# Kernel optimization log

Hardware: AMD Instinct MI355X
Metric: run time of the kernel (lower is better)

## Reference

```python
import jax, jax.numpy as jnp
import numpy as np

N_NODES = 100000
N_IN = 256
N_OUT = 64
N_EDGES = 1600000


def setup_inputs() -> dict:
    key = jax.random.key(0)
    k_x, k_w, k_b, k_v, k_r, k_c = jax.random.split(key, 6)
    x = jax.random.normal(k_x, (N_NODES, N_IN), dtype=jnp.float32)
    W = jax.random.normal(k_w, (N_IN, N_OUT), dtype=jnp.float32) * (1.0 / np.sqrt(N_IN))
    b = jax.random.normal(k_b, (N_OUT,), dtype=jnp.float32) * 0.01
    adj_vals = jax.random.uniform(k_v, (N_EDGES,), dtype=jnp.float32)
    edge_rows = jax.random.randint(k_r, (N_EDGES,), 0, N_NODES, dtype=jnp.int32)
    edge_cols = jax.random.randint(k_c, (N_EDGES,), 0, N_NODES, dtype=jnp.int32)
    return {"x": x, "W": W, "b": b, "adj_vals": adj_vals,
            "edge_rows": edge_rows, "edge_cols": edge_cols}


def reference(x, W, b, adj_vals, edge_rows, edge_cols):
    # linear projection: [N, n_in] @ [n_in, n_out] + b -> [N, n_out]
    h = x @ W + b
    # sparse-dense matmul: out[i] = sum_e adj_vals[e] * h[edge_cols[e]] for edge_rows[e]==i
    msgs = h[edge_cols] * adj_vals[:, None]  # [E, n_out]
    out = jax.ops.segment_sum(msgs, edge_rows, num_segments=N_NODES)
    return out
```

## Files before the change

### kernel.cpp

```cpp
#include <hip/hip_runtime.h>


#include <stdint.h>

constexpr int KDIM = 256;
constexpr int MOUT = 64;

constexpr int RPB = 128;
constexpr int RPB_SHIFT = 7;
constexpr int MAXBUCK = 1024;
constexpr int CHUNK = 8192;
constexpr int COL_BITS = 20;
constexpr int COL_MASK = (1 << COL_BITS) - 1;
constexpr int SORT_CAP = 6144;

typedef __attribute__((ext_vector_type(8))) short short8v;
typedef __attribute__((ext_vector_type(4))) float f32x4;

__device__ __forceinline__ unsigned short f2bf(float f) {
  unsigned u = __float_as_uint(f);
  return (unsigned short)((u + 0x7fffu + ((u >> 16) & 1u)) >> 16);
}

__global__ __launch_bounds__(256)
void wt_transpose(const float* __restrict__ W, unsigned short* __restrict__ wt) {
  int n = blockIdx.x;
  int k = threadIdx.x;
  wt[n * KDIM + k] = f2bf(W[(size_t)k * MOUT + n]);
}

__global__ __launch_bounds__(256)
void gemm_mfma(const float* __restrict__ x, const unsigned short* __restrict__ wt,
               const float* __restrict__ bvec, unsigned short* __restrict__ h, int N) {
  __shared__ unsigned short wlds[MOUT][264];

  const int t = threadIdx.x;
  for (int i = t; i < MOUT * 32; i += 256) {
    int n = i >> 5, seg = i & 31;
    uint4 v = *reinterpret_cast<const uint4*>(&wt[n * KDIM + seg * 8]);
    *reinterpret_cast<uint4*>(&wlds[n][seg * 8]) = v;
  }
  __syncthreads();

  const int wave = t >> 6, lane = t & 63;
  const int lo = lane & 15, hi = lane >> 4;
  const int rowbase = blockIdx.x * 128 + wave * 32;

  float bias[4];
#pragma unroll
  for (int nt = 0; nt < 4; ++nt) bias[nt] = bvec[nt * 16 + lo];

  f32x4 acc[2][4] = {};

#pragma unroll
  for (int ks = 0; ks < 8; ++ks) {
    short8v bfr[4];
#pragma unroll
    for (int nt = 0; nt < 4; ++nt)
      bfr[nt] = *reinterpret_cast<const short8v*>(&wlds[nt * 16 + lo][ks * 32 + hi * 8]);
#pragma unroll
    for (int mr = 0; mr < 2; ++mr) {
      int r = rowbase + mr * 16 + lo;
      if (r >= N) r = N - 1;
      const float* xp = &x[(size_t)r * KDIM + ks * 32 + hi * 8];
      float4 p0 = *reinterpret_cast<const float4*>(xp);
      float4 p1 = *reinterpret_cast<const float4*>(xp + 4);
      short8v a;
      a[0] = (short)f2bf(p0.x); a[1] = (short)f2bf(p0.y);
      a[2] = (short)f2bf(p0.z); a[3] = (short)f2bf(p0.w);
      a[4] = (short)f2bf(p1.x); a[5] = (short)f2bf(p1.y);
      a[6] = (short)f2bf(p1.z); a[7] = (short)f2bf(p1.w);
#pragma unroll
      for (int nt = 0; nt < 4; ++nt)
        acc[mr][nt] = __builtin_amdgcn_mfma_f32_16x16x32_bf16(a, bfr[nt], acc[mr][nt], 0, 0, 0);
    }
  }

#pragma unroll
  for (int mr = 0; mr < 2; ++mr)
#pragma unroll
    for (int reg = 0; reg < 4; ++reg) {
      int row = rowbase + mr * 16 + hi * 4 + reg;
      if (row < N) {
#pragma unroll
        for (int nt = 0; nt < 4; ++nt)
          h[(size_t)row * MOUT + nt * 16 + lo] = f2bf(acc[mr][nt][reg] + bias[nt]);
      }
    }
}

__global__ __launch_bounds__(256)
void bucket_hist(const int* __restrict__ rows, int* __restrict__ bcnt, int E, int nbuck) {
  __shared__ int cnt[MAXBUCK];
  for (int i = threadIdx.x; i < nbuck; i += 256) cnt[i] = 0;
  __syncthreads();
  for (int e = blockIdx.x * 256 + threadIdx.x; e < E; e += gridDim.x * 256)
    atomicAdd(&cnt[rows[e] >> RPB_SHIFT], 1);
  __syncthreads();
  for (int i = threadIdx.x; i < nbuck; i += 256)
    if (cnt[i]) atomicAdd(&bcnt[i], cnt[i]);
}

__global__ __launch_bounds__(1024)
void scan_buckets(const int* __restrict__ bcnt, int* __restrict__ bptr,
                  int* __restrict__ bcur, int nbuck, int E) {
  __shared__ int buf[1024];
  int t = threadIdx.x;
  int x = (t < nbuck) ? bcnt[t] : 0;
  buf[t] = x;
  __syncthreads();
#pragma unroll
  for (int off = 1; off < 1024; off <<= 1) {
    int v = (t >= off) ? buf[t - off] : 0;
    __syncthreads();
    buf[t] += v;
    __syncthreads();
  }
  if (t < nbuck) {
    int ex = buf[t] - x;
    bptr[t] = ex;
    bcur[t] = ex;
  }
  if (t == 0) bptr[nbuck] = E;
}

__global__ __launch_bounds__(256)
void bucket_scatter(const int* __restrict__ rows, const int* __restrict__ cols,
                    const float* __restrict__ vals, int* __restrict__ bcur,
                    int2* __restrict__ sorted, int E, int nbuck) {
  __shared__ int lcnt[MAXBUCK];
  __shared__ int lbase[MAXBUCK];
  const int t = threadIdx.x;
  const int e0 = blockIdx.x * CHUNK;
  const int e1 = min(e0 + CHUNK, E);

  for (int i = t; i < nbuck; i += 256) lcnt[i] = 0;
  __syncthreads();
  for (int e = e0 + t; e < e1; e += 256)
    atomicAdd(&lcnt[rows[e] >> RPB_SHIFT], 1);
  __syncthreads();
  for (int i = t; i < nbuck; i += 256) {
    int c = lcnt[i];
    lbase[i] = c ? atomicAdd(&bcur[i], c) : 0;
  }
  __syncthreads();
  for (int i = t; i < nbuck; i += 256) lcnt[i] = 0;
  __syncthreads();
  for (int e = e0 + t; e < e1; e += 256) {
    int r = rows[e];
    int b = r >> RPB_SHIFT;
    int lrow = r & (RPB - 1);
    int pos = lbase[b] + atomicAdd(&lcnt[b], 1);
    sorted[pos] = make_int2((lrow << COL_BITS) | cols[e], __float_as_int(vals[e]));
  }
}

__global__ __launch_bounds__(256)
void bucket_sort(int2* __restrict__ sorted, const int* __restrict__ bptr,
                 int* __restrict__ row_ptr, int* __restrict__ bflag,
                 int N, int E, int nbuck) {
  __shared__ int2 eds[SORT_CAP];
  __shared__ int lcnt[RPB];
  __shared__ int loff[RPB];
  __shared__ int lcur[RPB];
  const int t = threadIdx.x;
  const int b = blockIdx.x;
  const int s = bptr[b];
  const int e = bptr[b + 1];
  const int cnt = e - s;
  const int row0 = b << RPB_SHIFT;

  if (b == 0 && t == 0) row_ptr[N] = E;

  if (cnt > SORT_CAP) {
    if (t == 0) bflag[b] = 1;
    if (t < RPB && row0 + t < N) row_ptr[row0 + t] = s;
    return;
  }
  if (t == 0) bflag[b] = 0;

  if (t < RPB) lcnt[t] = 0;
  __syncthreads();
  for (int j = s + t; j < e; j += 256) {
    int2 p = sorted[j];
    eds[j - s] = p;
    atomicAdd(&lcnt[p.x >> COL_BITS], 1);
  }
  __syncthreads();
  if (t < RPB) loff[t] = lcnt[t];
  __syncthreads();
  for (int off = 1; off < RPB; off <<= 1) {
    int v = (t < RPB && t >= off) ? loff[t - off] : 0;
    __syncthreads();
    if (t < RPB) loff[t] += v;
    __syncthreads();
  }
  if (t < RPB) {
    int ex = loff[t] - lcnt[t];
    loff[t] = ex;
    lcur[t] = 0;
    int grow = row0 + t;
    if (grow < N) row_ptr[grow] = s + ex;
  }
  __syncthreads();
  for (int idx = t; idx < cnt; idx += 256) {
    int2 p = eds[idx];
    int lr = p.x >> COL_BITS;
    int pos = s + loff[lr] + atomicAdd(&lcur[lr], 1);
    sorted[pos] = p;
  }
}

__device__ __forceinline__ void edge_fma(float* acc, const unsigned short* h,
                                         int2 p, int part) {
  float v = __int_as_float(p.y);
  int col = p.x & COL_MASK;
  uint4 hv = *reinterpret_cast<const uint4*>(&h[(size_t)col * MOUT + part * 8]);
  acc[0] += v * __uint_as_float(hv.x << 16);
  acc[1] += v * __uint_as_float(hv.x & 0xffff0000u);
  acc[2] += v * __uint_as_float(hv.y << 16);
  acc[3] += v * __uint_as_float(hv.y & 0xffff0000u);
  acc[4] += v * __uint_as_float(hv.z << 16);
  acc[5] += v * __uint_as_float(hv.z & 0xffff0000u);
  acc[6] += v * __uint_as_float(hv.w << 16);
  acc[7] += v * __uint_as_float(hv.w & 0xffff0000u);
}

__global__ __launch_bounds__(256)
void reduce_rows(const unsigned short* __restrict__ h, const int2* __restrict__ sorted,
                 const int* __restrict__ row_ptr, const int* __restrict__ bptr,
                 const int* __restrict__ bflag, float* __restrict__ out, int N) {
  int row = (blockIdx.x * 256 + threadIdx.x) >> 6;
  if (row >= N) return;
  int lane = threadIdx.x & 63;
  int slot = lane >> 3;
  int part = lane & 7;
  int b = row >> RPB_SHIFT;
  int lrow = row & (RPB - 1);
  bool filt = bflag[b] != 0;

  float acc[8];
#pragma unroll
  for (int i = 0; i < 8; ++i) acc[i] = 0.f;

  if (!filt) {
    int s = row_ptr[row];
    int e = row_ptr[row + 1];
    int j = s + slot;
    for (; j + 8 < e; j += 16) {
      int2 p0 = sorted[j];
      int2 p1 = sorted[j + 8];
      float v0 = __int_as_float(p0.y);
      float v1 = __int_as_float(p1.y);
      const uint4* a0 = reinterpret_cast<const uint4*>(
          &h[(size_t)(p0.x & COL_MASK) * MOUT + part * 8]);
      const uint4* a1 = reinterpret_cast<const uint4*>(
          &h[(size_t)(p1.x & COL_MASK) * MOUT + part * 8]);
      uint4 h0 = *a0;
      uint4 h1 = *a1;
      acc[0] += v0 * __uint_as_float(h0.x << 16);
      acc[1] += v0 * __uint_as_float(h0.x & 0xffff0000u);
      acc[2] += v0 * __uint_as_float(h0.y << 16);
      acc[3] += v0 * __uint_as_float(h0.y & 0xffff0000u);
      acc[4] += v0 * __uint_as_float(h0.z << 16);
      acc[5] += v0 * __uint_as_float(h0.z & 0xffff0000u);
      acc[6] += v0 * __uint_as_float(h0.w << 16);
      acc[7] += v0 * __uint_as_float(h0.w & 0xffff0000u);
      acc[0] += v1 * __uint_as_float(h1.x << 16);
      acc[1] += v1 * __uint_as_float(h1.x & 0xffff0000u);
      acc[2] += v1 * __uint_as_float(h1.y << 16);
      acc[3] += v1 * __uint_as_float(h1.y & 0xffff0000u);
      acc[4] += v1 * __uint_as_float(h1.z << 16);
      acc[5] += v1 * __uint_as_float(h1.z & 0xffff0000u);
      acc[6] += v1 * __uint_as_float(h1.w << 16);
      acc[7] += v1 * __uint_as_float(h1.w & 0xffff0000u);
    }
    if (j < e) edge_fma(acc, h, sorted[j], part);
  } else {
    int s = bptr[b];
    int e = bptr[b + 1];
    for (int j = s + slot; j < e; j += 8) {
      int2 p = sorted[j];
      if ((p.x >> COL_BITS) != lrow) continue;
      edge_fma(acc, h, p, part);
    }
  }

#pragma unroll
  for (int m = 8; m <= 32; m <<= 1)
#pragma unroll
    for (int i = 0; i < 8; ++i)
      acc[i] += __shfl_xor(acc[i], m, 64);

  if (slot == 0) {
    float* op = &out[(size_t)row * MOUT + part * 8];
    *reinterpret_cast<float4*>(op)     = make_float4(acc[0], acc[1], acc[2], acc[3]);
    *reinterpret_cast<float4*>(op + 4) = make_float4(acc[4], acc[5], acc[6], acc[7]);
  }
}

__global__ __launch_bounds__(256)
void scatter_edges(const unsigned short* __restrict__ h, const float* __restrict__ vals,
                   const int* __restrict__ rows, const int* __restrict__ cols,
                   float* __restrict__ out, int E) {
  long long idx = (long long)blockIdx.x * blockDim.x + threadIdx.x;
  int e = (int)(idx >> 4);
  int part = (int)(idx & 15);
  if (e >= E) return;
  int r = rows[e];
  int c = cols[e];
  float v = vals[e];
  uint2 hv = *reinterpret_cast<const uint2*>(&h[(size_t)c * MOUT + part * 4]);
  float* op = &out[(size_t)r * MOUT + part * 4];
  atomicAdd(op + 0, v * __uint_as_float(hv.x << 16));
  atomicAdd(op + 1, v * __uint_as_float(hv.x & 0xffff0000u));
  atomicAdd(op + 2, v * __uint_as_float(hv.y << 16));
  atomicAdd(op + 3, v * __uint_as_float(hv.y & 0xffff0000u));
}

static inline size_t align256(size_t x) { return (x + 255) & ~(size_t)255; }

extern "C" void kernel_launch(void* const* d_in, const int* in_sizes, int n_in,
                              void* d_out, int out_size, void* d_ws, size_t ws_size,
                              hipStream_t stream) {
  const float* x    = (const float*)d_in[0];
  const float* W    = (const float*)d_in[1];
  const float* bvec = (const float*)d_in[2];
  const float* vals = (const float*)d_in[3];
  const int* erows  = (const int*)d_in[4];
  const int* ecols  = (const int*)d_in[5];
  float* out = (float*)d_out;

  const int N = in_sizes[0] / KDIM;
  const int E = in_sizes[3];
  const int nbuck = (N + RPB - 1) / RPB;

  char* ws = (char*)d_ws;
  size_t off_h  = 0;
  size_t off_wt = align256(off_h + (size_t)N * MOUT * sizeof(short));
  size_t off_bp = align256(off_wt + (size_t)MOUT * KDIM * sizeof(short));
  size_t off_bc = align256(off_bp + (size_t)(nbuck + 1) * sizeof(int));
  size_t off_cu = align256(off_bc + (size_t)nbuck * sizeof(int));
  size_t off_bf = align256(off_cu + (size_t)nbuck * sizeof(int));
  size_t off_rp = align256(off_bf + (size_t)nbuck * sizeof(int));
  size_t off_sp = align256(off_rp + (size_t)(N + 1) * sizeof(int));
  size_t need   = off_sp + (size_t)E * sizeof(int2);

  unsigned short* h  = (unsigned short*)(ws + off_h);
  unsigned short* wt = (unsigned short*)(ws + off_wt);

  dim3 blk256(256);
  wt_transpose<<<dim3(MOUT), blk256, 0, stream>>>(W, wt);
  gemm_mfma<<<dim3((N + 127) / 128), blk256, 0, stream>>>(x, wt, bvec, h, N);

  if (ws_size >= need && nbuck <= MAXBUCK && N < (1 << COL_BITS)) {
    int* bptr  = (int*)(ws + off_bp);
    int* bcnt  = (int*)(ws + off_bc);
    int* bcur  = (int*)(ws + off_cu);
    int* bflag = (int*)(ws + off_bf);
    int* row_ptr = (int*)(ws + off_rp);
    int2* sorted = (int2*)(ws + off_sp);

    hipMemsetAsync(bcnt, 0, (size_t)nbuck * sizeof(int), stream);
    bucket_hist<<<dim3(256), blk256, 0, stream>>>(erows, bcnt, E, nbuck);
    scan_buckets<<<dim3(1), dim3(1024), 0, stream>>>(bcnt, bptr, bcur, nbuck, E);
    bucket_scatter<<<dim3((E + CHUNK - 1) / CHUNK), blk256, 0, stream>>>(
        erows, ecols, vals, bcur, sorted, E, nbuck);
    bucket_sort<<<dim3(nbuck), blk256, 0, stream>>>(sorted, bptr, row_ptr, bflag, N, E, nbuck);
    reduce_rows<<<dim3(((size_t)N * 64 + 255) / 256), blk256, 0, stream>>>(
        h, sorted, row_ptr, bptr, bflag, out, N);
  } else {
    hipMemsetAsync(d_out, 0, (size_t)out_size * sizeof(float), stream);
    long long work = (long long)E * 16;
    scatter_edges<<<dim3((unsigned)((work + 255) / 256)), blk256, 0, stream>>>(h, vals, erows, ecols, out, E);
  }
}
```

Before: 144.5 us.

## Fuse weight transpose into histogram kernel and GEMM into bucket scatter launch

The W transpose is merged into the bucket histogram kernel as extra blocks, and the MFMA projection GEMM is merged with the edge bucket scatter into one launch, with blocks picking their role by index and sharing one LDS buffer. This removes two kernel launches and lets the compute-heavy GEMM blocks run alongside the memory-bound scatter blocks. The scan kernel is also generalized to loop over chunks of 1024 buckets. The cost is higher LDS use per block for the scatter role and uneven work across block roles.

```diff
diff --git a/kernel.cpp b/kernel.cpp
--- a/kernel.cpp
+++ b/kernel.cpp
@@ -13,6 +13,7 @@
 constexpr int COL_BITS = 20;
 constexpr int COL_MASK = (1 << COL_BITS) - 1;
 constexpr int SORT_CAP = 6144;
+constexpr int HIST_BLOCKS = 256;
 
 typedef __attribute__((ext_vector_type(8))) short short8v;
 typedef __attribute__((ext_vector_type(4))) float f32x4;
@@ -23,81 +24,22 @@
 }
 
 __global__ __launch_bounds__(256)
-void wt_transpose(const float* __restrict__ W, unsigned short* __restrict__ wt) {
-  int n = blockIdx.x;
-  int k = threadIdx.x;
-  wt[n * KDIM + k] = f2bf(W[(size_t)k * MOUT + n]);
-}
-
-__global__ __launch_bounds__(256)
-void gemm_mfma(const float* __restrict__ x, const unsigned short* __restrict__ wt,
-               const float* __restrict__ bvec, unsigned short* __restrict__ h, int N) {
-  __shared__ unsigned short wlds[MOUT][264];
-
+void prep(const float* __restrict__ W, unsigned short* __restrict__ wt,
+          const int* __restrict__ rows, int* __restrict__ bcnt, int E, int nbuck) {
   const int t = threadIdx.x;
-  for (int i = t; i < MOUT * 32; i += 256) {
-    int n = i >> 5, seg = i & 31;
-    uint4 v = *reinterpret_cast<const uint4*>(&wt[n * KDIM + seg * 8]);
-    *reinterpret_cast<uint4*>(&wlds[n][seg * 8]) = v;
-  }
-  __syncthreads();
-
-  const int wave = t >> 6, lane = t & 63;
-  const int lo = lane & 15, hi = lane >> 4;
-  const int rowbase = blockIdx.x * 128 + wave * 32;
-
-  float bias[4];
-#pragma unroll
-  for (int nt = 0; nt < 4; ++nt) bias[nt] = bvec[nt * 16 + lo];
-
-  f32x4 acc[2][4] = {};
-
-#pragma unroll
-  for (int ks = 0; ks < 8; ++ks) {
-    short8v bfr[4];
-#pragma unroll
-    for (int nt = 0; nt < 4; ++nt)
-      bfr[nt] = *reinterpret_cast<const short8v*>(&wlds[nt * 16 + lo][ks * 32 + hi * 8]);
-#pragma unroll
-    for (int mr = 0; mr < 2; ++mr) {
-      int r = rowbase + mr * 16 + lo;
-      if (r >= N) r = N - 1;
-      const float* xp = &x[(size_t)r * KDIM + ks * 32 + hi * 8];
-      float4 p0 = *reinterpret_cast<const float4*>(xp);
-      float4 p1 = *reinterpret_cast<const float4*>(xp + 4);
-      short8v a;
-      a[0] = (short)f2bf(p0.x); a[1] = (short)f2bf(p0.y);
-      a[2] = (short)f2bf(p0.z); a[3] = (short)f2bf(p0.w);
-      a[4] = (short)f2bf(p1.x); a[5] = (short)f2bf(p1.y);
-      a[6] = (short)f2bf(p1.z); a[7] = (short)f2bf(p1.w);
-#pragma unroll
-      for (int nt = 0; nt < 4; ++nt)
-        acc[mr][nt] = __builtin_amdgcn_mfma_f32_16x16x32_bf16(a, bfr[nt], acc[mr][nt], 0, 0, 0);
-    }
-  }
-
-#pragma unroll
-  for (int mr = 0; mr < 2; ++mr)
-#pragma unroll
-    for (int reg = 0; reg < 4; ++reg) {
-      int row = rowbase + mr * 16 + hi * 4 + reg;
-      if (row < N) {
-#pragma unroll
-        for (int nt = 0; nt < 4; ++nt)
-          h[(size_t)row * MOUT + nt * 16 + lo] = f2bf(acc[mr][nt][reg] + bias[nt]);
-      }
-    }
-}
-
-__global__ __launch_bounds__(256)
-void bucket_hist(const int* __restrict__ rows, int* __restrict__ bcnt, int E, int nbuck) {
+  if ((int)blockIdx.x < 64) {
+    int n = blockIdx.x;
+    wt[n * KDIM + t] = f2bf(W[(size_t)t * MOUT + n]);
+    return;
+  }
   __shared__ int cnt[MAXBUCK];
-  for (int i = threadIdx.x; i < nbuck; i += 256) cnt[i] = 0;
-  __syncthreads();
-  for (int e = blockIdx.x * 256 + threadIdx.x; e < E; e += gridDim.x * 256)
+  for (int i = t; i < nbuck; i += 256) cnt[i] = 0;
+  __syncthreads();
+  const int b0 = blockIdx.x - 64;
+  for (int e = b0 * 256 + t; e < E; e += HIST_BLOCKS * 256)
     atomicAdd(&cnt[rows[e] >> RPB_SHIFT], 1);
   __syncthreads();
-  for (int i = threadIdx.x; i < nbuck; i += 256)
+  for (int i = t; i < nbuck; i += 256)
     if (cnt[i]) atomicAdd(&bcnt[i], cnt[i]);
 }
 
@@ -105,33 +47,105 @@
 void scan_buckets(const int* __restrict__ bcnt, int* __restrict__ bptr,
                   int* __restrict__ bcur, int nbuck, int E) {
   __shared__ int buf[1024];
-  int t = threadIdx.x;
-  int x = (t < nbuck) ? bcnt[t] : 0;
-  buf[t] = x;
-  __syncthreads();
-#pragma unroll
-  for (int off = 1; off < 1024; off <<= 1) {
-    int v = (t >= off) ? buf[t - off] : 0;
-    __syncthreads();
-    buf[t] += v;
-    __syncthreads();
-  }
-  if (t < nbuck) {
-    int ex = buf[t] - x;
-    bptr[t] = ex;
-    bcur[t] = ex;
+  __shared__ int carry;
+  const int t = threadIdx.x;
+  if (t == 0) carry = 0;
+  __syncthreads();
+  for (int c0 = 0; c0 < nbuck; c0 += 1024) {
+    int i = c0 + t;
+    int x = (i < nbuck) ? bcnt[i] : 0;
+    buf[t] = x;
+    __syncthreads();
+    for (int off = 1; off < 1024; off <<= 1) {
+      int v = (t >= off) ? buf[t - off] : 0;
+      __syncthreads();
+      buf[t] += v;
+      __syncthreads();
+    }
+    int incl = buf[t];
+    int base = carry;
+    if (i < nbuck) {
+      int ex = base + incl - x;
+      bptr[i] = ex;
+      bcur[i] = ex;
+    }
+    __syncthreads();
+    if (t == 1023) carry = base + incl;
+    __syncthreads();
   }
   if (t == 0) bptr[nbuck] = E;
 }
 
 __global__ __launch_bounds__(256)
-void bucket_scatter(const int* __restrict__ rows, const int* __restrict__ cols,
-                    const float* __restrict__ vals, int* __restrict__ bcur,
-                    int2* __restrict__ sorted, int E, int nbuck) {
-  __shared__ int lcnt[MAXBUCK];
-  __shared__ int lbase[MAXBUCK];
+void gemm_scatter(const float* __restrict__ x, const unsigned short* __restrict__ wt,
+                  const float* __restrict__ bvec, unsigned short* __restrict__ h,
+                  const int* __restrict__ rows, const int* __restrict__ cols,
+                  const float* __restrict__ vals, int* __restrict__ bcur,
+                  int2* __restrict__ sorted, int gemmBlocks, int N, int E, int nbuck) {
+  __shared__ __align__(16) char smem[MOUT * 264 * 2];
   const int t = threadIdx.x;
-  const int e0 = blockIdx.x * CHUNK;
+
+  if ((int)blockIdx.x < gemmBlocks) {
+    auto wlds = reinterpret_cast<unsigned short(*)[264]>(smem);
+    for (int i = t; i < MOUT * 32; i += 256) {
+      int n = i >> 5, seg = i & 31;
+      uint4 v = *reinterpret_cast<const uint4*>(&wt[n * KDIM + seg * 8]);
+      *reinterpret_cast<uint4*>(&wlds[n][seg * 8]) = v;
+    }
+    __syncthreads();
+
+    const int wave = t >> 6, lane = t & 63;
+    const int lo = lane & 15, hi = lane >> 4;
+    const int rowbase = blockIdx.x * 128 + wave * 32;
+
+    float bias[4];
+#pragma unroll
+    for (int nt = 0; nt < 4; ++nt) bias[nt] = bvec[nt * 16 + lo];
+
+    f32x4 acc[2][4] = {};
+
+#pragma unroll
+    for (int ks = 0; ks < 8; ++ks) {
+      short8v bfr[4];
+#pragma unroll
+      for (int nt = 0; nt < 4; ++nt)
+        bfr[nt] = *reinterpret_cast<const short8v*>(&wlds[nt * 16 + lo][ks * 32 + hi * 8]);
+#pragma unroll
+      for (int mr = 0; mr < 2; ++mr) {
+        int r = rowbase + mr * 16 + lo;
+        if (r >= N) r = N - 1;
+        const float* xp = &x[(size_t)r * KDIM + ks * 32 + hi * 8];
+        float4 p0 = *reinterpret_cast<const float4*>(xp);
+        float4 p1 = *reinterpret_cast<const float4*>(xp + 4);
+        short8v a;
+        a[0] = (short)f2bf(p0.x); a[1] = (short)f2bf(p0.y);
+        a[2] = (short)f2bf(p0.z); a[3] = (short)f2bf(p0.w);
+        a[4] = (short)f2bf(p1.x); a[5] = (short)f2bf(p1.y);
+        a[6] = (short)f2bf(p1.z); a[7] = (short)f2bf(p1.w);
+#pragma unroll
+        for (int nt = 0; nt < 4; ++nt)
+          acc[mr][nt] = __builtin_amdgcn_mfma_f32_16x16x32_bf16(a, bfr[nt], acc[mr][nt], 0, 0, 0);
+      }
+    }
+
+#pragma unroll
+    for (int mr = 0; mr < 2; ++mr)
+#pragma unroll
+      for (int reg = 0; reg < 4; ++reg) {
+        int row = rowbase + mr * 16 + hi * 4 + reg;
+        if (row < N) {
+#pragma unroll
+          for (int nt = 0; nt < 4; ++nt)
+            h[(size_t)row * MOUT + nt * 16 + lo] = f2bf(acc[mr][nt][reg] + bias[nt]);
+        }
+      }
+    return;
+  }
+
+  int* lcnt  = reinterpret_cast<int*>(smem);
+  int* lbase = lcnt + MAXBUCK;
+  const int cid = blockIdx.x - gemmBlocks;
+  const int e0 = cid * CHUNK;
   const int e1 = min(e0 + CHUNK, E);
 
   for (int i = t; i < nbuck; i += 256) lcnt[i] = 0;
@@ -252,12 +266,10 @@
       int2 p1 = sorted[j + 8];
       float v0 = __int_as_float(p0.y);
       float v1 = __int_as_float(p1.y);
-      const uint4* a0 = reinterpret_cast<const uint4*>(
+      uint4 h0 = *reinterpret_cast<const uint4*>(
           &h[(size_t)(p0.x & COL_MASK) * MOUT + part * 8]);
-      const uint4* a1 = reinterpret_cast<const uint4*>(
+      uint4 h1 = *reinterpret_cast<const uint4*>(
           &h[(size_t)(p1.x & COL_MASK) * MOUT + part * 8]);
-      uint4 h0 = *a0;
-      uint4 h1 = *a1;
       acc[0] += v0 * __uint_as_float(h0.x << 16);
       acc[1] += v0 * __uint_as_float(h0.x & 0xffff0000u);
       acc[2] += v0 * __uint_as_float(h0.y << 16);
@@ -318,6 +330,13 @@
   atomicAdd(op + 3, v * __uint_as_float(hv.y & 0xffff0000u));
 }
 
+__global__ __launch_bounds__(256)
+void wt_transpose(const float* __restrict__ W, unsigned short* __restrict__ wt) {
+  int n = blockIdx.x;
+  int k = threadIdx.x;
+  wt[n * KDIM + k] = f2bf(W[(size_t)k * MOUT + n]);
+}
+
 static inline size_t align256(size_t x) { return (x + 255) & ~(size_t)255; }
 
 extern "C" void kernel_launch(void* const* d_in, const int* in_sizes, int n_in,
@@ -350,8 +369,7 @@
   unsigned short* wt = (unsigned short*)(ws + off_wt);
 
   dim3 blk256(256);
-  wt_transpose<<<dim3(MOUT), blk256, 0, stream>>>(W, wt);
-  gemm_mfma<<<dim3((N + 127) / 128), blk256, 0, stream>>>(x, wt, bvec, h, N);
+  const int gemmBlocks = (N + 127) / 128;
 
   if (ws_size >= need && nbuck <= MAXBUCK && N < (1 << COL_BITS)) {
     int* bptr  = (int*)(ws + off_bp);
@@ -362,14 +380,18 @@
     int2* sorted = (int2*)(ws + off_sp);
 
     hipMemsetAsync(bcnt, 0, (size_t)nbuck * sizeof(int), stream);
-    bucket_hist<<<dim3(256), blk256, 0, stream>>>(erows, bcnt, E, nbuck);
+    prep<<<dim3(64 + HIST_BLOCKS), blk256, 0, stream>>>(W, wt, erows, bcnt, E, nbuck);
     scan_buckets<<<dim3(1), dim3(1024), 0, stream>>>(bcnt, bptr, bcur, nbuck, E);
-    bucket_scatter<<<dim3((E + CHUNK - 1) / CHUNK), blk256, 0, stream>>>(
-        erows, ecols, vals, bcur, sorted, E, nbuck);
+    const int scatBlocks = (E + CHUNK - 1) / CHUNK;
+    gemm_scatter<<<dim3(gemmBlocks + scatBlocks), blk256, 0, stream>>>(
+        x, wt, bvec, h, erows, ecols, vals, bcur, sorted, gemmBlocks, N, E, nbuck);
     bucket_sort<<<dim3(nbuck), blk256, 0, stream>>>(sorted, bptr, row_ptr, bflag, N, E, nbuck);
     reduce_rows<<<dim3(((size_t)N * 64 + 255) / 256), blk256, 0, stream>>>(
         h, sorted, row_ptr, bptr, bflag, out, N);
   } else {
+    wt_transpose<<<dim3(MOUT), blk256, 0, stream>>>(W, wt);
+    gemm_scatter<<<dim3(gemmBlocks), blk256, 0, stream>>>(
+        x, wt, bvec, h, erows, ecols, vals, (int*)wt, (int2*)h, gemmBlocks, N, E, nbuck);
     hipMemsetAsync(d_out, 0, (size_t)out_size * sizeof(float), stream);
     long long work = (long long)E * 16;
     scatter_edges<<<dim3((unsigned)((work + 255) / 256)), blk256, 0, stream>>>(h, vals, erows, ecols, out, E);
```

After: 127.9 us. 1.13x faster.
